# Kernel optimization log

Measured on AMD Instinct MI355X. Metric: run time of the kernel, lower is better.

Reference implementation:

```python
import jax, jax.numpy as jnp
import numpy as np

N, E, B, IN, H, T = 50000, 800000, 256, 32, 96, 8
BN_EPS = 1e-5


def setup_inputs() -> dict:
    key = jax.random.key(0)
    ks = jax.random.split(key, 40)
    inp = {}
    inp["x"] = jax.random.normal(ks[0], (N, IN), dtype=jnp.float32)
    inp["edge_index"] = jax.random.randint(ks[1], (2, E), 0, N, dtype=jnp.int64)
    inp["batch"] = jnp.sort(jax.random.randint(ks[2], (N,), 0, B, dtype=jnp.int64))
    inp["r_target"] = jax.random.randint(ks[3], (B,), 0, T, dtype=jnp.int64)
    k = 4
    for i, din in zip((1, 2, 3), (IN, H, H)):
        inp[f"w_in{i}"] = jax.random.normal(ks[k], (din, H), dtype=jnp.float32) / np.sqrt(din); k += 1
        inp[f"b_in{i}"] = jnp.zeros((H,), dtype=jnp.float32)
        inp[f"gamma{i}"] = jnp.ones((H,), dtype=jnp.float32)
        inp[f"beta{i}"] = jnp.zeros((H,), dtype=jnp.float32)
        inp[f"rmean{i}"] = jax.random.normal(ks[k], (H,), dtype=jnp.float32) * 0.1; k += 1
        inp[f"rvar{i}"] = jax.random.uniform(ks[k], (H,), minval=0.5, maxval=1.5, dtype=jnp.float32); k += 1
        inp[f"w_out{i}"] = jax.random.normal(ks[k], (H, H), dtype=jnp.float32) / np.sqrt(H); k += 1
        inp[f"b_out{i}"] = jnp.zeros((H,), dtype=jnp.float32)
    inp["head_w"] = jax.random.normal(ks[k], (T, H), dtype=jnp.float32) / np.sqrt(H)
    inp["head_b"] = jnp.zeros((T,), dtype=jnp.float32)
    return inp


def gin_conv(h, edge_index, w_in, b_in, gamma, beta, rmean, rvar, w_out, b_out):
    # PyG GINConv with eps=0: mlp((1+0)*x + sum_{j in N(i)} x_j)
    agg = jax.ops.segment_sum(h[edge_index[0]], edge_index[1], num_segments=N)
    z = (h + agg) @ w_in + b_in                                   # [N, H]
    z = (z - rmean) * (gamma * jax.lax.rsqrt(rvar + BN_EPS)) + beta  # eval-mode BN
    z = jax.nn.relu(z)
    z = jax.nn.relu(z @ w_out + b_out)
    return z


def reference(x, edge_index, batch, r_target,
              w_in1, b_in1, gamma1, beta1, rmean1, rvar1, w_out1, b_out1,
              w_in2, b_in2, gamma2, beta2, rmean2, rvar2, w_out2, b_out2,
              w_in3, b_in3, gamma3, beta3, rmean3, rvar3, w_out3, b_out3,
              head_w, head_b):
    h = gin_conv(x, edge_index, w_in1, b_in1, gamma1, beta1, rmean1, rvar1, w_out1, b_out1)
    h = jax.nn.relu(h)
    h = gin_conv(h, edge_index, w_in2, b_in2, gamma2, beta2, rmean2, rvar2, w_out2, b_out2)
    h = jax.nn.relu(h)
    h = gin_conv(h, edge_index, w_in3, b_in3, gamma3, beta3, rmean3, rvar3, w_out3, b_out3)
    pooled = jax.ops.segment_sum(h, batch, num_segments=B)        # [B, H]
    # dropout p=0.5 in eval mode -> identity
    w = head_w[r_target]                                          # [B, H] per-sample head
    b = head_b[r_target]                                          # [B]
    return jnp.sum(pooled * w, axis=-1) + b                       # [B]
```

## Files before the change

### kernel.cpp

```cpp
#include <hip/hip_runtime.h>

using u16 = unsigned short;
using u32 = unsigned int;

typedef __attribute__((ext_vector_type(8))) short bf16x8;
typedef __attribute__((ext_vector_type(4))) float f32x4;

constexpr int Nn  = 50000;
constexpr int Ee  = 800000;
constexpr int Bb  = 256;
constexpr int INF = 32;
constexpr int Hh  = 96;
constexpr float BN_EPS = 1e-5f;

constexpr int BINW = 256;
constexpr int NBIN = (Nn + BINW - 1) / BINW;
constexpr int P1B  = 256;
constexpr int EPB  = Ee / P1B;
constexpr int CAP  = 64;

constexpr int WROW   = 104;
constexpr int WMAT   = 96 * WROW;
constexpr int WB_TOT = 6 * WMAT;

__device__ __forceinline__ float bfL(u32 u) { return __uint_as_float(u << 16); }
__device__ __forceinline__ float bfH(u32 u) { return __uint_as_float(u & 0xFFFF0000u); }
__device__ __forceinline__ u32 f2bfb(float f) {
    u32 b = __float_as_uint(f);
    return (b + 0x7FFFu + ((b >> 16) & 1u)) >> 16;
}
__device__ __forceinline__ float bf2f(u16 u) { return __uint_as_float(((u32)u) << 16); }

__global__ void x2bf_kernel(const float* __restrict__ x, u16* __restrict__ xb) {
    const int total = Nn * INF / 8;
    for (int i = blockIdx.x * 256 + threadIdx.x; i < total; i += gridDim.x * 256) {
        const float4 a = ((const float4*)x)[2 * i];
        const float4 b = ((const float4*)x)[2 * i + 1];
        uint4 R;
        R.x = f2bfb(a.x) | (f2bfb(a.y) << 16);
        R.y = f2bfb(a.z) | (f2bfb(a.w) << 16);
        R.z = f2bfb(b.x) | (f2bfb(b.y) << 16);
        R.w = f2bfb(b.z) | (f2bfb(b.w) << 16);
        ((uint4*)xb)[i] = R;
    }
}

__global__ void w2bf_kernel(const float* __restrict__ w1i, const float* __restrict__ w1o,
                            const float* __restrict__ w2i, const float* __restrict__ w2o,
                            const float* __restrict__ w3i, const float* __restrict__ w3o,
                            u16* __restrict__ wb) {
    const int i = blockIdx.x * 256 + threadIdx.x;
    if (i >= WB_TOT / 2) return;
    const int mat = i / (WMAT / 2);
    const int rem = i % (WMAT / 2);
    const int j   = rem / (WROW / 2);
    const int k   = (rem % (WROW / 2)) * 2;
    const float* src; int din;
    switch (mat) {
        case 0: src = w1i; din = 32; break;
        case 1: src = w1o; din = 96; break;
        case 2: src = w2i; din = 96; break;
        case 3: src = w2o; din = 96; break;
        case 4: src = w3i; din = 96; break;
        default: src = w3o; din = 96; break;
    }
    const u32 lo = (k     < din) ? f2bfb(src[(long)k * 96 + j])       : 0u;
    const u32 hi = (k + 1 < din) ? f2bfb(src[(long)(k + 1) * 96 + j]) : 0u;
    ((u32*)wb)[i] = lo | (hi << 16);
}

__global__ __launch_bounds__(256)
void p1_bin_kernel(const int* __restrict__ src, const int* __restrict__ dst,
                   u32* __restrict__ binbuf, int* __restrict__ counts) {
    __shared__ int cur[NBIN];
    const int b = blockIdx.x, tid = threadIdx.x;
    for (int k = tid; k < NBIN; k += 256) cur[k] = 0;
    __syncthreads();
    const long e0 = (long)b * EPB;
    for (int i = tid; i < EPB; i += 256) {
        const long e = e0 + i;
        const int d = dst[e];
        const int k = d >> 8;
        const int pos = atomicAdd(&cur[k], 1);
        binbuf[((long)b * NBIN + k) * CAP + pos] = ((u32)(d & 255) << 16) | (u32)src[e];
    }
    __syncthreads();
    for (int k = tid; k < NBIN; k += 256) counts[k * P1B + b] = cur[k];
}

__global__ void p2_binscan_kernel(const int* __restrict__ counts, int* __restrict__ binbase,
                                  int* __restrict__ rowptr) {
    __shared__ int ps[256];
    const int t = threadIdx.x;
    int tot = 0;
    if (t < NBIN) {
        const int* cp = counts + t * P1B;
        for (int b = 0; b < P1B; ++b) tot += cp[b];
    }
    ps[t] = tot;
    __syncthreads();
    for (int d = 1; d < 256; d <<= 1) {
        int u = (t >= d) ? ps[t - d] : 0;
        __syncthreads();
        if (t >= d) ps[t] += u;
        __syncthreads();
    }
    if (t < NBIN) binbase[t] = ps[t] - tot;
    if (t == 0) rowptr[Nn] = Ee;
}

__global__ __launch_bounds__(256)
void p3_binsort_kernel(const u32* __restrict__ binbuf, const int* __restrict__ counts,
                       const int* __restrict__ binbase, int* __restrict__ rowptr,
                       u16* __restrict__ csr) {
    __shared__ int cnt[P1B];
    __shared__ int lhist[BINW];
    __shared__ int lpref[BINW];
    const int k = blockIdx.x, tid = threadIdx.x;

    for (int b = tid; b < P1B; b += 256) cnt[b] = counts[k * P1B + b];
    lhist[tid] = 0;
    __syncthreads();

    for (int flat = tid; flat < P1B * CAP; flat += 256) {
        const int b = flat / CAP, i = flat % CAP;
        if (i < cnt[b])
            atomicAdd(&lhist[binbuf[((long)b * NBIN + k) * CAP + i] >> 16], 1);
    }
    __syncthreads();

    const int v = lhist[tid];
    lpref[tid] = v;
    __syncthreads();
    for (int d = 1; d < 256; d <<= 1) {
        int u = (tid >= d) ? lpref[tid - d] : 0;
        __syncthreads();
        if (tid >= d) lpref[tid] += u;
        __syncthreads();
    }
    lpref[tid] -= v;

    const int base = binbase[k];
    const int node = k * BINW + tid;
    if (node < Nn) rowptr[node] = base + lpref[tid];
    lhist[tid] = 0;
    __syncthreads();

    for (int flat = tid; flat < P1B * CAP; flat += 256) {
        const int b = flat / CAP, i = flat % CAP;
        if (i < cnt[b]) {
            const u32 pv = binbuf[((long)b * NBIN + k) * CAP + i];
            const int dl = pv >> 16;
            const int pos = base + lpref[dl] + atomicAdd(&lhist[dl], 1);
            csr[pos] = (u16)(pv & 0xFFFFu);
        }
    }
}

template<int DIN>
__global__ __launch_bounds__(384, 4)
void layer_kernel(const u16* __restrict__ hsrc, const int* __restrict__ rowptr,
                  const u16* __restrict__ csr,
                  const u16* __restrict__ wbg1, const u16* __restrict__ wbg2,
                  const float* __restrict__ b_in,
                  const float* __restrict__ gamma, const float* __restrict__ beta,
                  const float* __restrict__ rmean, const float* __restrict__ rvar,
                  const float* __restrict__ b_out,
                  u16* __restrict__ out) {
    constexpr int TILE = 32;
    constexpr int XST  = 104;
    __shared__ __align__(16) u16 wT[96 * XST];
    __shared__ __align__(16) u16 xs[TILE * XST];

    const int tid = threadIdx.x;
    const int nbase = blockIdx.x * TILE;

    for (int i = tid; i < 96 * XST / 8; i += 384)
        ((uint4*)wT)[i] = ((const uint4*)wbg1)[i];

    {
        const int grp = tid / 12, ln = tid % 12;
        const int node = nbase + grp;
        if (node < Nn) {
            const int e0 = rowptr[node], e1 = rowptr[node + 1];
            if constexpr (DIN == 96) {
                const uint4* h4 = (const uint4*)hsrc;
                float a0, a1, a2, a3, a4, a5, a6, a7;
                {
                    const uint4 U = h4[(long)node * 12 + ln];
                    a0 = bfL(U.x); a1 = bfH(U.x); a2 = bfL(U.y); a3 = bfH(U.y);
                    a4 = bfL(U.z); a5 = bfH(U.z); a6 = bfL(U.w); a7 = bfH(U.w);
                }
                int e = e0;
                for (; e + 4 <= e1; e += 4) {
                    const long s0 = csr[e], s1 = csr[e + 1], s2 = csr[e + 2], s3 = csr[e + 3];
                    const uint4 U0 = h4[s0 * 12 + ln];
                    const uint4 U1 = h4[s1 * 12 + ln];
                    const uint4 U2 = h4[s2 * 12 + ln];
                    const uint4 U3 = h4[s3 * 12 + ln];
                    a0 += bfL(U0.x); a1 += bfH(U0.x); a2 += bfL(U0.y); a3 += bfH(U0.y);
                    a4 += bfL(U0.z); a5 += bfH(U0.z); a6 += bfL(U0.w); a7 += bfH(U0.w);
                    a0 += bfL(U1.x); a1 += bfH(U1.x); a2 += bfL(U1.y); a3 += bfH(U1.y);
                    a4 += bfL(U1.z); a5 += bfH(U1.z); a6 += bfL(U1.w); a7 += bfH(U1.w);
                    a0 += bfL(U2.x); a1 += bfH(U2.x); a2 += bfL(U2.y); a3 += bfH(U2.y);
                    a4 += bfL(U2.z); a5 += bfH(U2.z); a6 += bfL(U2.w); a7 += bfH(U2.w);
                    a0 += bfL(U3.x); a1 += bfH(U3.x); a2 += bfL(U3.y); a3 += bfH(U3.y);
                    a4 += bfL(U3.z); a5 += bfH(U3.z); a6 += bfL(U3.w); a7 += bfH(U3.w);
                }
                for (; e < e1; ++e) {
                    const uint4 U = h4[(long)csr[e] * 12 + ln];
                    a0 += bfL(U.x); a1 += bfH(U.x); a2 += bfL(U.y); a3 += bfH(U.y);
                    a4 += bfL(U.z); a5 += bfH(U.z); a6 += bfL(U.w); a7 += bfH(U.w);
                }
                u32* xp = (u32*)&xs[grp * XST + ln * 8];
                xp[0] = f2bfb(a0) | (f2bfb(a1) << 16);
                xp[1] = f2bfb(a2) | (f2bfb(a3) << 16);
                xp[2] = f2bfb(a4) | (f2bfb(a5) << 16);
                xp[3] = f2bfb(a6) | (f2bfb(a7) << 16);
            } else {
                if (ln < 8) {
                    const uint2* h2 = (const uint2*)hsrc;
                    float a0, a1, a2, a3;
                    {
                        const uint2 U = h2[(long)node * 8 + ln];
                        a0 = bfL(U.x); a1 = bfH(U.x); a2 = bfL(U.y); a3 = bfH(U.y);
                    }
                    int e = e0;
                    for (; e + 4 <= e1; e += 4) {
                        const long s0 = csr[e], s1 = csr[e + 1], s2 = csr[e + 2], s3 = csr[e + 3];
                        const uint2 U0 = h2[s0 * 8 + ln];
                        const uint2 U1 = h2[s1 * 8 + ln];
                        const uint2 U2 = h2[s2 * 8 + ln];
                        const uint2 U3 = h2[s3 * 8 + ln];
                        a0 += bfL(U0.x); a1 += bfH(U0.x); a2 += bfL(U0.y); a3 += bfH(U0.y);
                        a0 += bfL(U1.x); a1 += bfH(U1.x); a2 += bfL(U1.y); a3 += bfH(U1.y);
                        a0 += bfL(U2.x); a1 += bfH(U2.x); a2 += bfL(U2.y); a3 += bfH(U2.y);
                        a0 += bfL(U3.x); a1 += bfH(U3.x); a2 += bfL(U3.y); a3 += bfH(U3.y);
                    }
                    for (; e < e1; ++e) {
                        const uint2 U = h2[(long)csr[e] * 8 + ln];
                        a0 += bfL(U.x); a1 += bfH(U.x); a2 += bfL(U.y); a3 += bfH(U.y);
                    }
                    u32* xp = (u32*)&xs[grp * XST + ln * 4];
                    xp[0] = f2bfb(a0) | (f2bfb(a1) << 16);
                    xp[1] = f2bfb(a2) | (f2bfb(a3) << 16);
                }
            }
        } else {
            if constexpr (DIN == 96) {
                u32* xp = (u32*)&xs[grp * XST + ln * 8];
                xp[0] = xp[1] = xp[2] = xp[3] = 0u;
            } else if (ln < 8) {
                u32* q = (u32*)&xs[grp * XST + ln * 4];
                q[0] = q[1] = 0u;
            }
        }
    }

    const int lane = tid & 63, wave = tid >> 6;
    const int lr = lane & 15;
    const int md = (lane >> 4) * 4;
    const int lk = (lane >> 4) * 8;
    const int jg = wave * 16 + lr;

    const float sA = gamma[jg] * rsqrtf(rvar[jg] + BN_EPS);
    const float sC = (b_in[jg] - rmean[jg]) * sA + beta[jg];
    const float Bo = b_out[jg];
    __syncthreads();

    f32x4 acc0 = {0.f, 0.f, 0.f, 0.f}, acc1 = {0.f, 0.f, 0.f, 0.f};
    #pragma unroll
    for (int ks = 0; ks < DIN / 32; ++ks) {
        const int k0 = ks * 32 + lk;
        const bf16x8 b  = *(const bf16x8*)&wT[jg * XST + k0];
        const bf16x8 a0 = *(const bf16x8*)&xs[lr * XST + k0];
        const bf16x8 a1 = *(const bf16x8*)&xs[(16 + lr) * XST + k0];
        acc0 = __builtin_amdgcn_mfma_f32_16x16x32_bf16(a0, b, acc0, 0, 0, 0);
        acc1 = __builtin_amdgcn_mfma_f32_16x16x32_bf16(a1, b, acc1, 0, 0, 0);
    }

    u16 z0[4], z1[4];
    #pragma unroll
    for (int r = 0; r < 4; ++r) {
        z0[r] = (u16)f2bfb(fmaxf(fmaf(acc0[r], sA, sC), 0.0f));
        z1[r] = (u16)f2bfb(fmaxf(fmaf(acc1[r], sA, sC), 0.0f));
    }
    __syncthreads();

    #pragma unroll
    for (int r = 0; r < 4; ++r) {
        xs[(md + r) * XST + jg]      = z0[r];
        xs[(16 + md + r) * XST + jg] = z1[r];
    }
    for (int i = tid; i < 96 * XST / 8; i += 384)
        ((uint4*)wT)[i] = ((const uint4*)wbg2)[i];
    __syncthreads();

    f32x4 o0 = {0.f, 0.f, 0.f, 0.f}, o1 = {0.f, 0.f, 0.f, 0.f};
    #pragma unroll
    for (int ks = 0; ks < 3; ++ks) {
        const int k0 = ks * 32 + lk;
        const bf16x8 b  = *(const bf16x8*)&wT[jg * XST + k0];
        const bf16x8 a0 = *(const bf16x8*)&xs[lr * XST + k0];
        const bf16x8 a1 = *(const bf16x8*)&xs[(16 + lr) * XST + k0];
        o0 = __builtin_amdgcn_mfma_f32_16x16x32_bf16(a0, b, o0, 0, 0, 0);
        o1 = __builtin_amdgcn_mfma_f32_16x16x32_bf16(a1, b, o1, 0, 0, 0);
    }

    #pragma unroll
    for (int r = 0; r < 4; ++r) {
        const int n0 = nbase + md + r;
        if (n0 < Nn)
            out[(long)n0 * Hh + jg] = (u16)f2bfb(fmaxf(o0[r] + Bo, 0.0f));
        const int n1 = nbase + 16 + md + r;
        if (n1 < Nn)
            out[(long)n1 * Hh + jg] = (u16)f2bfb(fmaxf(o1[r] + Bo, 0.0f));
    }
}

constexpr int PCHUNK = 64;
__global__ void pool_kernel(const u16* __restrict__ h, const int* __restrict__ batch,
                            float* __restrict__ pooled) {
    const int j = threadIdx.x;
    const int c0 = blockIdx.x * PCHUNK;
    const int c1 = min(c0 + PCHUNK, Nn);
    if (c0 >= Nn) return;

    int bcur = batch[c0];
    float acc = 0.0f;
    for (int n = c0; n < c1; ++n) {
        const int bb = batch[n];
        if (bb != bcur) {
            atomicAdd(&pooled[(long)bcur * Hh + j], acc);
            acc = 0.0f;
            bcur = bb;
        }
        acc += bf2f(h[(long)n * Hh + j]);
    }
    atomicAdd(&pooled[(long)bcur * Hh + j], acc);
}

__global__ void head_kernel(const float* __restrict__ pooled, const int* __restrict__ rt,
                            const float* __restrict__ hw, const float* __restrict__ hb,
                            float* __restrict__ outv) {
    const int b = blockIdx.x;
    const int lane = threadIdx.x;
    const int t = rt[b];
    const float* pp = pooled + (long)b * Hh;
    const float* wp = hw + (long)t * Hh;
    float s = 0.0f;
    for (int j = lane; j < Hh; j += 64) s += pp[j] * wp[j];
    #pragma unroll
    for (int off = 32; off > 0; off >>= 1) s += __shfl_down(s, off, 64);
    if (lane == 0) outv[b] = s + hb[t];
}

extern "C" void kernel_launch(void* const* d_in, const int* in_sizes, int n_in,
                              void* d_out, int out_size, void* d_ws, size_t ws_size,
                              hipStream_t stream) {
    const float* x     = (const float*)d_in[0];
    const int*   ei    = (const int*)d_in[1];
    const int*   src   = ei;
    const int*   dst   = ei + Ee;
    const int*   batch = (const int*)d_in[2];
    const int*   rt    = (const int*)d_in[3];

    const float* P[3][8];
    for (int l = 0; l < 3; ++l)
        for (int p = 0; p < 8; ++p)
            P[l][p] = (const float*)d_in[4 + l * 8 + p];
    const float* head_w = (const float*)d_in[28];
    const float* head_b = (const float*)d_in[29];

    const size_t NH = (size_t)Nn * Hh;
    u16*   tA      = (u16*)d_ws;
    u16*   tB      = tA + NH;
    u16*   xb      = tB + NH;
    u16*   wball   = xb + (size_t)Nn * INF;
    float* pooled  = (float*)(wball + WB_TOT);
    int*   rowptr  = (int*)(pooled + (size_t)Bb * Hh);
    int*   counts  = rowptr + Nn + 1;
    int*   binbase = counts + NBIN * P1B;
    u16*   csr     = (u16*)(binbase + NBIN);
    u32*   binbuf  = (u32*)tA;
    float* out     = (float*)d_out;

    const dim3 blk256(256), blk384(384), blk96(96);
    const int GRID_L    = (Nn + 31) / 32;
    const int GRID_POOL = (Nn + PCHUNK - 1) / PCHUNK;

    x2bf_kernel<<<782, blk256, 0, stream>>>(x, xb);
    w2bf_kernel<<<(WB_TOT / 2 + 255) / 256, blk256, 0, stream>>>(
        P[0][0], P[0][6], P[1][0], P[1][6], P[2][0], P[2][6], wball);
    p1_bin_kernel<<<P1B, blk256, 0, stream>>>(src, dst, binbuf, counts);
    p2_binscan_kernel<<<1, blk256, 0, stream>>>(counts, binbase, rowptr);
    p3_binsort_kernel<<<NBIN, blk256, 0, stream>>>(binbuf, counts, binbase, rowptr, csr);

    layer_kernel<INF><<<GRID_L, blk384, 0, stream>>>(xb, rowptr, csr,
        wball + 0 * WMAT, wball + 1 * WMAT,
        P[0][1], P[0][2], P[0][3], P[0][4], P[0][5], P[0][7], tA);

    layer_kernel<Hh><<<GRID_L, blk384, 0, stream>>>(tA, rowptr, csr,
        wball + 2 * WMAT, wball + 3 * WMAT,
        P[1][1], P[1][2], P[1][3], P[1][4], P[1][5], P[1][7], tB);

    layer_kernel<Hh><<<GRID_L, blk384, 0, stream>>>(tB, rowptr, csr,
        wball + 4 * WMAT, wball + 5 * WMAT,
        P[2][1], P[2][2], P[2][3], P[2][4], P[2][5], P[2][7], tA);

    hipMemsetAsync(pooled, 0, (size_t)Bb * Hh * sizeof(float), stream);
    pool_kernel<<<GRID_POOL, blk96, 0, stream>>>(tA, batch, pooled);
    head_kernel<<<Bb, 64, 0, stream>>>(pooled, rt, head_w, head_b, out);
}
```

Baseline: 179.2 us.

## Narrow CSR bins, atomically total bin counts, cache binned edges in registers

Halves the destination-bin width to 128 nodes, which doubles the number of bins and therefore the number of binsort blocks, and shrinks per-bin capacity to 40. Per-bin totals are now accumulated with global atomics in the binning kernel, so the single-block scan no longer serially sums 256 counts per bin. The binsort kernel keeps each thread's packed edges in registers between the histogram pass and the scatter pass instead of reading binbuf twice. The risks are overflow if any block-bin receives more than 40 edges, and the added memset and atomic traffic.

```diff
diff --git a/kernel.cpp b/kernel.cpp
--- a/kernel.cpp
+++ b/kernel.cpp
@@ -2,6 +2,7 @@
 
 using u16 = unsigned short;
 using u32 = unsigned int;
+using u64 = unsigned long long;
 
 typedef __attribute__((ext_vector_type(8))) short bf16x8;
 typedef __attribute__((ext_vector_type(4))) float f32x4;
@@ -13,11 +14,12 @@
 constexpr int Hh  = 96;
 constexpr float BN_EPS = 1e-5f;
 
-constexpr int BINW = 256;
+constexpr int BINW = 128;
 constexpr int NBIN = (Nn + BINW - 1) / BINW;
 constexpr int P1B  = 256;
 constexpr int EPB  = Ee / P1B;
-constexpr int CAP  = 64;
+constexpr int CAP  = 40;
+constexpr int P3IT = P1B * CAP / 256;
 
 constexpr int WROW   = 104;
 constexpr int WMAT   = 96 * WROW;
@@ -71,7 +73,8 @@
 
 __global__ __launch_bounds__(256)
 void p1_bin_kernel(const int* __restrict__ src, const int* __restrict__ dst,
-                   u32* __restrict__ binbuf, int* __restrict__ counts) {
+                   u32* __restrict__ binbuf, int* __restrict__ counts,
+                   int* __restrict__ bintot) {
     __shared__ int cur[NBIN];
     const int b = blockIdx.x, tid = threadIdx.x;
     for (int k = tid; k < NBIN; k += 256) cur[k] = 0;
@@ -80,32 +83,32 @@
     for (int i = tid; i < EPB; i += 256) {
         const long e = e0 + i;
         const int d = dst[e];
-        const int k = d >> 8;
+        const int k = d >> 7;
         const int pos = atomicAdd(&cur[k], 1);
-        binbuf[((long)b * NBIN + k) * CAP + pos] = ((u32)(d & 255) << 16) | (u32)src[e];
-    }
-    __syncthreads();
-    for (int k = tid; k < NBIN; k += 256) counts[k * P1B + b] = cur[k];
-}
-
-__global__ void p2_binscan_kernel(const int* __restrict__ counts, int* __restrict__ binbase,
+        binbuf[((long)b * NBIN + k) * CAP + pos] = ((u32)(d & 127) << 16) | (u32)src[e];
+    }
+    __syncthreads();
+    for (int k = tid; k < NBIN; k += 256) {
+        const int c = cur[k];
+        counts[k * P1B + b] = c;
+        if (c) atomicAdd(&bintot[k], c);
+    }
+}
+
+__global__ void p2_binscan_kernel(const int* __restrict__ bintot, int* __restrict__ binbase,
                                   int* __restrict__ rowptr) {
-    __shared__ int ps[256];
+    __shared__ int ps[512];
     const int t = threadIdx.x;
-    int tot = 0;
-    if (t < NBIN) {
-        const int* cp = counts + t * P1B;
-        for (int b = 0; b < P1B; ++b) tot += cp[b];
-    }
-    ps[t] = tot;
-    __syncthreads();
-    for (int d = 1; d < 256; d <<= 1) {
+    const int v = (t < NBIN) ? bintot[t] : 0;
+    ps[t] = v;
+    __syncthreads();
+    for (int d = 1; d < 512; d <<= 1) {
         int u = (t >= d) ? ps[t - d] : 0;
         __syncthreads();
         if (t >= d) ps[t] += u;
         __syncthreads();
     }
-    if (t < NBIN) binbase[t] = ps[t] - tot;
+    if (t < NBIN) binbase[t] = ps[t] - v;
     if (t == 0) rowptr[Nn] = Ee;
 }
 
@@ -119,40 +122,48 @@
     const int k = blockIdx.x, tid = threadIdx.x;
 
     for (int b = tid; b < P1B; b += 256) cnt[b] = counts[k * P1B + b];
-    lhist[tid] = 0;
-    __syncthreads();
-
-    for (int flat = tid; flat < P1B * CAP; flat += 256) {
+    if (tid < BINW) lhist[tid] = 0;
+    __syncthreads();
+
+    u32 pv[P3IT];
+    u64 vmask = 0;
+    #pragma unroll
+    for (int it = 0; it < P3IT; ++it) {
+        const int flat = tid + it * 256;
         const int b = flat / CAP, i = flat % CAP;
-        if (i < cnt[b])
-            atomicAdd(&lhist[binbuf[((long)b * NBIN + k) * CAP + i] >> 16], 1);
-    }
-    __syncthreads();
-
-    const int v = lhist[tid];
-    lpref[tid] = v;
-    __syncthreads();
-    for (int d = 1; d < 256; d <<= 1) {
-        int u = (tid >= d) ? lpref[tid - d] : 0;
+        if (i < cnt[b]) {
+            const u32 v = binbuf[((long)b * NBIN + k) * CAP + i];
+            pv[it] = v;
+            vmask |= 1ull << it;
+            atomicAdd(&lhist[v >> 16], 1);
+        }
+    }
+    __syncthreads();
+
+    if (tid < BINW) lpref[tid] = lhist[tid];
+    __syncthreads();
+    for (int d = 1; d < BINW; d <<= 1) {
+        int u = 0;
+        if (tid < BINW && tid >= d) u = lpref[tid - d];
         __syncthreads();
-        if (tid >= d) lpref[tid] += u;
+        if (tid < BINW && tid >= d) lpref[tid] += u;
         __syncthreads();
     }
-    lpref[tid] -= v;
+    if (tid < BINW) lpref[tid] -= lhist[tid];
 
     const int base = binbase[k];
     const int node = k * BINW + tid;
-    if (node < Nn) rowptr[node] = base + lpref[tid];
-    lhist[tid] = 0;
-    __syncthreads();
-
-    for (int flat = tid; flat < P1B * CAP; flat += 256) {
-        const int b = flat / CAP, i = flat % CAP;
-        if (i < cnt[b]) {
-            const u32 pv = binbuf[((long)b * NBIN + k) * CAP + i];
-            const int dl = pv >> 16;
+    if (tid < BINW && node < Nn) rowptr[node] = base + lpref[tid];
+    if (tid < BINW) lhist[tid] = 0;
+    __syncthreads();
+
+    #pragma unroll
+    for (int it = 0; it < P3IT; ++it) {
+        if (vmask & (1ull << it)) {
+            const u32 v = pv[it];
+            const int dl = v >> 16;
             const int pos = base + lpref[dl] + atomicAdd(&lhist[dl], 1);
-            csr[pos] = (u16)(pv & 0xFFFFu);
+            csr[pos] = (u16)(v & 0xFFFFu);
         }
     }
 }
@@ -381,19 +392,21 @@
     int*   rowptr  = (int*)(pooled + (size_t)Bb * Hh);
     int*   counts  = rowptr + Nn + 1;
     int*   binbase = counts + NBIN * P1B;
-    u16*   csr     = (u16*)(binbase + NBIN);
+    int*   bintot  = binbase + NBIN;
+    u16*   csr     = (u16*)(bintot + NBIN);
     u32*   binbuf  = (u32*)tA;
     float* out     = (float*)d_out;
 
-    const dim3 blk256(256), blk384(384), blk96(96);
+    const dim3 blk256(256), blk384(384), blk512(512), blk96(96);
     const int GRID_L    = (Nn + 31) / 32;
     const int GRID_POOL = (Nn + PCHUNK - 1) / PCHUNK;
 
     x2bf_kernel<<<782, blk256, 0, stream>>>(x, xb);
     w2bf_kernel<<<(WB_TOT / 2 + 255) / 256, blk256, 0, stream>>>(
         P[0][0], P[0][6], P[1][0], P[1][6], P[2][0], P[2][6], wball);
-    p1_bin_kernel<<<P1B, blk256, 0, stream>>>(src, dst, binbuf, counts);
-    p2_binscan_kernel<<<1, blk256, 0, stream>>>(counts, binbase, rowptr);
+    hipMemsetAsync(bintot, 0, NBIN * sizeof(int), stream);
+    p1_bin_kernel<<<P1B, blk256, 0, stream>>>(src, dst, binbuf, counts, bintot);
+    p2_binscan_kernel<<<1, blk512, 0, stream>>>(bintot, binbase, rowptr);
     p3_binsort_kernel<<<NBIN, blk256, 0, stream>>>(binbuf, counts, binbase, rowptr, csr);
 
     layer_kernel<INF><<<GRID_L, blk384, 0, stream>>>(xb, rowptr, csr,
```

New measurement: 167.4 us. 6.6% less time.
